# Kernel tuning notes

Hardware: AMD Instinct MI355X
Metric: run time of the kernel (lower is better)

The kernel has to match this reference:

```python
import jax, jax.numpy as jnp
import numpy as np

TEMP = 1.0  # unique_3D_act_temperature
EPS = 1e-10


def _trilinear_border(vol, gx, gy, gz):
    """grid_sample 5D, mode=bilinear (trilinear), padding=border, align_corners=True.
    vol: [C, D, H, W]; gx/gy/gz: [P] normalized coords in [-1, 1] (x->W, y->H, z->D).
    Returns [C, P]."""
    C, D, H, W = vol.shape
    fx = jnp.clip((gx + 1.0) * 0.5 * (W - 1), 0.0, W - 1)
    fy = jnp.clip((gy + 1.0) * 0.5 * (H - 1), 0.0, H - 1)
    fz = jnp.clip((gz + 1.0) * 0.5 * (D - 1), 0.0, D - 1)
    x0 = jnp.floor(fx).astype(jnp.int32); x1 = jnp.minimum(x0 + 1, W - 1)
    y0 = jnp.floor(fy).astype(jnp.int32); y1 = jnp.minimum(y0 + 1, H - 1)
    z0 = jnp.floor(fz).astype(jnp.int32); z1 = jnp.minimum(z0 + 1, D - 1)
    wx = fx - x0; wy = fy - y0; wz = fz - z0
    def g(zi, yi, xi):
        return vol[:, zi, yi, xi]  # [C, P] gather
    c00 = g(z0, y0, x0) * (1 - wx) + g(z0, y0, x1) * wx
    c01 = g(z0, y1, x0) * (1 - wx) + g(z0, y1, x1) * wx
    c10 = g(z1, y0, x0) * (1 - wx) + g(z1, y0, x1) * wx
    c11 = g(z1, y1, x0) * (1 - wx) + g(z1, y1, x1) * wx
    c0 = c00 * (1 - wy) + c01 * wy
    c1 = c10 * (1 - wy) + c11 * wy
    return c0 * (1 - wz) + c1 * wz


def setup_inputs() -> dict:
    key = jax.random.key(0)
    k1, k2, k3, k4 = jax.random.split(key, 4)
    B, NR, NS = 1, 8192, 128
    Cdim, Ddim, Hd, Wd = 1, 256, 240, 320
    H, W = 480, 640
    fx_, fy_, cx, cy = 500.0, 500.0, W / 2.0, H / 2.0
    intr = jnp.array([[[fx_, 0.0, cx], [0.0, fy_, cy], [0.0, 0.0, 1.0]]], dtype=jnp.float32)
    # back-project random pixels at random depths so projections fall mostly in frame
    u = jax.random.uniform(k1, (B, NR, NS), minval=0.0, maxval=float(W))
    v = jax.random.uniform(k2, (B, NR, NS), minval=0.0, maxval=float(H))
    z = jax.random.uniform(k3, (B, NR, NS), minval=1.1, maxval=10.0)
    pts = jnp.stack([(u - cx) / fx_ * z, (v - cy) / fy_ * z, z], axis=-1).astype(jnp.float32)
    feature_volume = 0.01 * jax.random.normal(k4, (1, Cdim, Ddim, Hd, Wd), dtype=jnp.float32)
    learnable_max_value = 5.0 * jnp.ones((1, 1, 1, Hd, Wd), dtype=jnp.float32)
    return {"feature_volume": feature_volume, "learnable_max_value": learnable_max_value,
            "intr": intr, "points_3D_samples": pts,
            "H": H, "W": W, "depth_min": 0, "depth_max": 1}


def reference(feature_volume, learnable_max_value, intr, points_3D_samples, H, W, depth_min, depth_max):
    B, NR, NS, _ = points_3D_samples.shape
    Cdim = feature_volume.shape[1]
    # camera projection: points @ intr^T
    p2d = jnp.einsum('bnsk,bjk->bnsj', points_3D_samples, intr)
    px, py, pz = p2d[..., 0], p2d[..., 1], p2d[..., 2]
    gx = (px / (pz + EPS) / W - 0.5) * 2.0
    gy = (py / (pz + EPS) / H - 0.5) * 2.0
    gz = ((1.0 / pz - depth_min) / (depth_max - depth_min) - 0.5) * 2.0
    # unique_3D_act density: softmax over depth axis * (relu(max) + 0.01)
    density = jax.nn.softmax(feature_volume * TEMP, axis=2) * (jax.nn.relu(learnable_max_value) + 0.01)
    vol = density[0]  # [C, D, Hd, Wd]
    feat = _trilinear_border(vol, gx.reshape(-1), gy.reshape(-1), gz.reshape(-1))  # [C, P]
    feat = feat.reshape(Cdim, B, NR, NS).transpose(1, 2, 3, 0)  # [B, NR, NS, C]
    density_samples = feat[..., 0]  # cdim == 1 -> squeeze(-1)
    return density_samples
```

## Files before the change

kernel.cpp:

```cpp
#include <hip/hip_runtime.h>
#include <hip/hip_fp16.h>
#include <math.h>

#define DD 256
#define HD 240
#define WD 320
#define HWPIX (HD * WD)
#define DCHUNK 16
#define NCHUNK (DD / DCHUNK)

union Quad {
    uint2 u;
    struct { __half2 lo, hi; } h;
};

__global__ __launch_bounds__(256) void k_rebuild_quad(
        const float* __restrict__ vol,
        uint2* __restrict__ quad,
        float* __restrict__ partial) {
    int pix = blockIdx.x * 256 + threadIdx.x;
    int d0 = blockIdx.y * DCHUNK;
    int y = pix / WD;
    int pixn = (y < HD - 1) ? pix + WD : pix;
    const float* p0 = vol + pix;
    const float* p1 = vol + pixn;

    float a[DCHUNK + 1], b[DCHUNK + 1];
#pragma unroll
    for (int j = 0; j <= DCHUNK; ++j) {
        int d = d0 + j; if (d > DD - 1) d = DD - 1;
        a[j] = p0[(size_t)d * HWPIX];
        b[j] = p1[(size_t)d * HWPIX];
    }
#pragma unroll
    for (int j = 0; j <= DCHUNK; ++j) { a[j] = __expf(a[j]); b[j] = __expf(b[j]); }

    float s0 = 0.f, s1 = 0.f;
#pragma unroll
    for (int j = 0; j < DCHUNK; j += 2) { s0 += a[j]; s1 += a[j + 1]; }

#pragma unroll
    for (int j = 0; j < DCHUNK; ++j) {
        Quad q;
        q.h.lo = __floats2half2_rn(a[j],     b[j]);
        q.h.hi = __floats2half2_rn(a[j + 1], b[j + 1]);
        quad[(size_t)(d0 + j) * HWPIX + pix] = q.u;
    }
    partial[blockIdx.y * HWPIX + pix] = s0 + s1;
}

__global__ __launch_bounds__(256) void k_stats_partial(
        const float* __restrict__ vol,
        float* __restrict__ partial) {
    int pix = blockIdx.x * 256 + threadIdx.x;
    int d0 = blockIdx.y * DCHUNK;
    const float* p = vol + pix;
    float v[DCHUNK];
#pragma unroll
    for (int j = 0; j < DCHUNK; ++j) v[j] = p[(size_t)(d0 + j) * HWPIX];
    float s0 = 0.f, s1 = 0.f;
#pragma unroll
    for (int j = 0; j < DCHUNK; j += 2) { s0 += __expf(v[j]); s1 += __expf(v[j + 1]); }
    partial[blockIdx.y * HWPIX + pix] = s0 + s1;
}

__global__ __launch_bounds__(256) void k_finalize(
        const float* __restrict__ partial,
        const float* __restrict__ lmax,
        float* __restrict__ coef) {
    int pix = blockIdx.x * 256 + threadIdx.x;
    float s = 0.f;
#pragma unroll
    for (int c = 0; c < NCHUNK; ++c) s += partial[c * HWPIX + pix];
    coef[pix] = (fmaxf(lmax[pix], 0.0f) + 0.01f) / s;
}

__device__ __forceinline__ void project(
        const float* __restrict__ intr, const float* __restrict__ pts, int i,
        float Himg, float Wimg, float dmin, float dmax,
        int& x0, int& x1, float& wx, int& y0, int& y1, float& wy,
        int& z0, float& wz) {
    float X = pts[3 * i + 0];
    float Y = pts[3 * i + 1];
    float Z = pts[3 * i + 2];
    float px = intr[0] * X + intr[1] * Y + intr[2] * Z;
    float py = intr[3] * X + intr[4] * Y + intr[5] * Z;
    float pz = intr[6] * X + intr[7] * Y + intr[8] * Z;
    float inv = 1.0f / (pz + 1e-10f);
    float gx = (px * inv / Wimg - 0.5f) * 2.0f;
    float gy = (py * inv / Himg - 0.5f) * 2.0f;
    float gz = ((1.0f / pz - dmin) / (dmax - dmin) - 0.5f) * 2.0f;
    float fx = fminf(fmaxf((gx + 1.0f) * 0.5f * (float)(WD - 1), 0.0f), (float)(WD - 1));
    float fy = fminf(fmaxf((gy + 1.0f) * 0.5f * (float)(HD - 1), 0.0f), (float)(HD - 1));
    float fz = fminf(fmaxf((gz + 1.0f) * 0.5f * (float)(DD - 1), 0.0f), (float)(DD - 1));
    x0 = (int)floorf(fx); x1 = min(x0 + 1, WD - 1); wx = fx - (float)x0;
    y0 = (int)floorf(fy); y1 = min(y0 + 1, HD - 1); wy = fy - (float)y0;
    z0 = (int)floorf(fz); wz = fz - (float)z0;
}

__device__ __forceinline__ float sample_one_quad(
        const uint2* __restrict__ quad, const float* __restrict__ coef,
        const float* __restrict__ intr, const float* __restrict__ pts,
        float Himg, float Wimg, float dmin, float dmax, int i) {
    int x0, x1, y0, y1, z0; float wx, wy, wz;
    project(intr, pts, i, Himg, Wimg, dmin, dmax, x0, x1, wx, y0, y1, wy, z0, wz);

    size_t base = (size_t)z0 * HWPIX + (size_t)y0 * WD;
    Quad qa, qb;
    qa.u = quad[base + x0];
    qb.u = quad[base + x1];
    float c00 = coef[y0 * WD + x0], c01 = coef[y0 * WD + x1];
    float c10 = coef[y1 * WD + x0], c11 = coef[y1 * WD + x1];

    float2 alo = __half22float2(qa.h.lo);
    float2 ahi = __half22float2(qa.h.hi);
    float2 blo = __half22float2(qb.h.lo);
    float2 bhi = __half22float2(qb.h.hi);

    float d000 = alo.x * c00, d010 = alo.y * c10;
    float d100 = ahi.x * c00, d110 = ahi.y * c10;
    float d001 = blo.x * c01, d011 = blo.y * c11;
    float d101 = bhi.x * c01, d111 = bhi.y * c11;

    float e00 = d000 * (1.0f - wx) + d001 * wx;
    float e01 = d010 * (1.0f - wx) + d011 * wx;
    float e10 = d100 * (1.0f - wx) + d101 * wx;
    float e11 = d110 * (1.0f - wx) + d111 * wx;
    float f0 = e00 * (1.0f - wy) + e01 * wy;
    float f1 = e10 * (1.0f - wy) + e11 * wy;
    return f0 * (1.0f - wz) + f1 * wz;
}

__global__ __launch_bounds__(256) void k_sample_quad(
        const uint2* __restrict__ quad,
        const float* __restrict__ coef,
        const float* __restrict__ intr,
        const float* __restrict__ pts,
        const int* __restrict__ Hp, const int* __restrict__ Wp,
        const int* __restrict__ dminp, const int* __restrict__ dmaxp,
        float* __restrict__ out, int P, int half) {
    int t = blockIdx.x * 256 + threadIdx.x;
    if (t >= half) return;
    float Himg = (float)(*Hp), Wimg = (float)(*Wp);
    float dmin = (float)(*dminp), dmax = (float)(*dmaxp);

    int i0 = t, i1 = t + half;
    float r0 = sample_one_quad(quad, coef, intr, pts, Himg, Wimg, dmin, dmax, i0);
    out[i0] = r0;
    if (i1 < P) {
        float r1 = sample_one_quad(quad, coef, intr, pts, Himg, Wimg, dmin, dmax, i1);
        out[i1] = r1;
    }
}

__global__ __launch_bounds__(256) void k_sample_vol(
        const float* __restrict__ vol,
        const float* __restrict__ coef,
        const float* __restrict__ intr,
        const float* __restrict__ pts,
        const int* __restrict__ Hp, const int* __restrict__ Wp,
        const int* __restrict__ dminp, const int* __restrict__ dmaxp,
        float* __restrict__ out, int P) {
    int i = blockIdx.x * 256 + threadIdx.x;
    if (i >= P) return;
    float Himg = (float)(*Hp), Wimg = (float)(*Wp);
    float dmin = (float)(*dminp), dmax = (float)(*dmaxp);
    int x0, x1, y0, y1, z0; float wx, wy, wz;
    project(intr, pts, i, Himg, Wimg, dmin, dmax, x0, x1, wx, y0, y1, wy, z0, wz);
    int z1 = min(z0 + 1, DD - 1);

    int p00 = y0 * WD + x0, p01 = y0 * WD + x1;
    int p10 = y1 * WD + x0, p11 = y1 * WD + x1;
    float c00 = coef[p00], c01 = coef[p01], c10 = coef[p10], c11 = coef[p11];
    const float* v0 = vol + (size_t)z0 * HWPIX;
    const float* v1 = vol + (size_t)z1 * HWPIX;

    float a00 = __expf(v0[p00]) * c00, a01 = __expf(v0[p01]) * c01;
    float a10 = __expf(v0[p10]) * c10, a11 = __expf(v0[p11]) * c11;
    float b00 = __expf(v1[p00]) * c00, b01 = __expf(v1[p01]) * c01;
    float b10 = __expf(v1[p10]) * c10, b11 = __expf(v1[p11]) * c11;

    float ax0 = a00 * (1.0f - wx) + a01 * wx;
    float ax1 = a10 * (1.0f - wx) + a11 * wx;
    float bx0 = b00 * (1.0f - wx) + b01 * wx;
    float bx1 = b10 * (1.0f - wx) + b11 * wx;
    float a = ax0 * (1.0f - wy) + ax1 * wy;
    float b = bx0 * (1.0f - wy) + bx1 * wy;
    out[i] = a * (1.0f - wz) + b * wz;
}

extern "C" void kernel_launch(void* const* d_in, const int* in_sizes, int n_in,
                              void* d_out, int out_size, void* d_ws, size_t ws_size,
                              hipStream_t stream) {
    const float* vol  = (const float*)d_in[0];
    const float* lmax = (const float*)d_in[1];
    const float* intr = (const float*)d_in[2];
    const float* pts  = (const float*)d_in[3];
    const int* Hp     = (const int*)d_in[4];
    const int* Wp     = (const int*)d_in[5];
    const int* dminp  = (const int*)d_in[6];
    const int* dmaxp  = (const int*)d_in[7];
    float* out = (float*)d_out;
    int P = out_size;

    const size_t quad_bytes = (size_t)DD * HWPIX * sizeof(uint2);
    const size_t part_bytes = (size_t)NCHUNK * HWPIX * 4;
    const size_t coef_bytes = (size_t)HWPIX * 4;

    dim3 blk(256);
    dim3 grd_rb(HWPIX / 256, NCHUNK);
    dim3 grd_fin(HWPIX / 256);

    if (ws_size >= quad_bytes + part_bytes + coef_bytes) {
        uint2* quad    = (uint2*)d_ws;
        float* partial = (float*)((char*)d_ws + quad_bytes);
        float* coef    = (float*)((char*)d_ws + quad_bytes + part_bytes);
        k_rebuild_quad<<<grd_rb, blk, 0, stream>>>(vol, quad, partial);
        k_finalize<<<grd_fin, blk, 0, stream>>>(partial, lmax, coef);
        int half = (P + 1) / 2;
        dim3 grd_smp((half + 255) / 256);
        k_sample_quad<<<grd_smp, blk, 0, stream>>>(quad, coef, intr, pts,
                                                   Hp, Wp, dminp, dmaxp, out, P, half);
    } else {
        float* partial = (float*)d_ws;
        float* coef    = (float*)((char*)d_ws + part_bytes);
        k_stats_partial<<<grd_rb, blk, 0, stream>>>(vol, partial);
        k_finalize<<<grd_fin, blk, 0, stream>>>(partial, lmax, coef);
        dim3 grd_smp((P + 255) / 256);
        k_sample_vol<<<grd_smp, blk, 0, stream>>>(vol, coef, intr, pts,
                                                  Hp, Wp, dminp, dmaxp, out, P);
    }
}
```

Baseline: 194.1 us.

## Pre-scale quad volume by softmax coefficients and sample four points per thread

Softmax statistics now come from a separate pass over the volume, and the fp16 quad volume is built afterwards with the normalisation coefficient already multiplied in. This lets the sampler skip the four coef gathers per point. The sampler now handles four consecutive points per thread with vectorized float4 loads of the points and a float4 store of the results. The cost is that the 78 MB fp32 volume is read twice (stats, then build) instead of once. Storing pre-scaled values in fp16 also changes rounding.

After: 207.6 us. 7.0% more time.

```diff
diff --git a/kernel.cpp b/kernel.cpp
--- a/kernel.cpp
+++ b/kernel.cpp
@@ -6,61 +6,28 @@
 #define HD 240
 #define WD 320
 #define HWPIX (HD * WD)
-#define DCHUNK 16
-#define NCHUNK (DD / DCHUNK)
+#define DC_S 32
+#define NC_S (DD / DC_S)
+#define DC_B 16
+#define NC_B (DD / DC_B)
 
 union Quad {
     uint2 u;
     struct { __half2 lo, hi; } h;
 };
 
-__global__ __launch_bounds__(256) void k_rebuild_quad(
-        const float* __restrict__ vol,
-        uint2* __restrict__ quad,
-        float* __restrict__ partial) {
-    int pix = blockIdx.x * 256 + threadIdx.x;
-    int d0 = blockIdx.y * DCHUNK;
-    int y = pix / WD;
-    int pixn = (y < HD - 1) ? pix + WD : pix;
-    const float* p0 = vol + pix;
-    const float* p1 = vol + pixn;
-
-    float a[DCHUNK + 1], b[DCHUNK + 1];
-#pragma unroll
-    for (int j = 0; j <= DCHUNK; ++j) {
-        int d = d0 + j; if (d > DD - 1) d = DD - 1;
-        a[j] = p0[(size_t)d * HWPIX];
-        b[j] = p1[(size_t)d * HWPIX];
-    }
-#pragma unroll
-    for (int j = 0; j <= DCHUNK; ++j) { a[j] = __expf(a[j]); b[j] = __expf(b[j]); }
-
-    float s0 = 0.f, s1 = 0.f;
-#pragma unroll
-    for (int j = 0; j < DCHUNK; j += 2) { s0 += a[j]; s1 += a[j + 1]; }
-
-#pragma unroll
-    for (int j = 0; j < DCHUNK; ++j) {
-        Quad q;
-        q.h.lo = __floats2half2_rn(a[j],     b[j]);
-        q.h.hi = __floats2half2_rn(a[j + 1], b[j + 1]);
-        quad[(size_t)(d0 + j) * HWPIX + pix] = q.u;
-    }
-    partial[blockIdx.y * HWPIX + pix] = s0 + s1;
-}
-
 __global__ __launch_bounds__(256) void k_stats_partial(
         const float* __restrict__ vol,
         float* __restrict__ partial) {
     int pix = blockIdx.x * 256 + threadIdx.x;
-    int d0 = blockIdx.y * DCHUNK;
+    int d0 = blockIdx.y * DC_S;
     const float* p = vol + pix;
-    float v[DCHUNK];
-#pragma unroll
-    for (int j = 0; j < DCHUNK; ++j) v[j] = p[(size_t)(d0 + j) * HWPIX];
+    float v[DC_S];
+#pragma unroll
+    for (int j = 0; j < DC_S; ++j) v[j] = p[(size_t)(d0 + j) * HWPIX];
     float s0 = 0.f, s1 = 0.f;
 #pragma unroll
-    for (int j = 0; j < DCHUNK; j += 2) { s0 += __expf(v[j]); s1 += __expf(v[j + 1]); }
+    for (int j = 0; j < DC_S; j += 2) { s0 += __expf(v[j]); s1 += __expf(v[j + 1]); }
     partial[blockIdx.y * HWPIX + pix] = s0 + s1;
 }
 
@@ -71,21 +38,52 @@
     int pix = blockIdx.x * 256 + threadIdx.x;
     float s = 0.f;
 #pragma unroll
-    for (int c = 0; c < NCHUNK; ++c) s += partial[c * HWPIX + pix];
+    for (int c = 0; c < NC_S; ++c) s += partial[c * HWPIX + pix];
     coef[pix] = (fmaxf(lmax[pix], 0.0f) + 0.01f) / s;
 }
 
-__device__ __forceinline__ void project(
-        const float* __restrict__ intr, const float* __restrict__ pts, int i,
+__global__ __launch_bounds__(256) void k_build_quad(
+        const float* __restrict__ vol,
+        const float* __restrict__ coef,
+        uint2* __restrict__ quad) {
+    int pix = blockIdx.x * 256 + threadIdx.x;
+    int d0 = blockIdx.y * DC_B;
+    int y = pix / WD;
+    int pixn = (y < HD - 1) ? pix + WD : pix;
+    const float* p0 = vol + pix;
+    const float* p1 = vol + pixn;
+    float c0 = coef[pix];
+    float c1 = coef[pixn];
+
+    float a[DC_B + 1], b[DC_B + 1];
+#pragma unroll
+    for (int j = 0; j <= DC_B; ++j) {
+        int d = d0 + j; if (d > DD - 1) d = DD - 1;
+        a[j] = p0[(size_t)d * HWPIX];
+        b[j] = p1[(size_t)d * HWPIX];
+    }
+#pragma unroll
+    for (int j = 0; j <= DC_B; ++j) {
+        a[j] = __expf(a[j]) * c0;
+        b[j] = __expf(b[j]) * c1;
+    }
+#pragma unroll
+    for (int j = 0; j < DC_B; ++j) {
+        Quad q;
+        q.h.lo = __floats2half2_rn(a[j],     b[j]);
+        q.h.hi = __floats2half2_rn(a[j + 1], b[j + 1]);
+        quad[(size_t)(d0 + j) * HWPIX + pix] = q.u;
+    }
+}
+
+__device__ __forceinline__ void project_idx(
+        float X, float Y, float Z,
+        float i00, float i02, float i11, float i12,
         float Himg, float Wimg, float dmin, float dmax,
-        int& x0, int& x1, float& wx, int& y0, int& y1, float& wy,
-        int& z0, float& wz) {
-    float X = pts[3 * i + 0];
-    float Y = pts[3 * i + 1];
-    float Z = pts[3 * i + 2];
-    float px = intr[0] * X + intr[1] * Y + intr[2] * Z;
-    float py = intr[3] * X + intr[4] * Y + intr[5] * Z;
-    float pz = intr[6] * X + intr[7] * Y + intr[8] * Z;
+        size_t& base, int& x0, int& x1, float& wx, float& wy, float& wz) {
+    float px = i00 * X + i02 * Z;
+    float py = i11 * Y + i12 * Z;
+    float pz = Z;
     float inv = 1.0f / (pz + 1e-10f);
     float gx = (px * inv / Wimg - 0.5f) * 2.0f;
     float gy = (py * inv / Himg - 0.5f) * 2.0f;
@@ -94,62 +92,101 @@
     float fy = fminf(fmaxf((gy + 1.0f) * 0.5f * (float)(HD - 1), 0.0f), (float)(HD - 1));
     float fz = fminf(fmaxf((gz + 1.0f) * 0.5f * (float)(DD - 1), 0.0f), (float)(DD - 1));
     x0 = (int)floorf(fx); x1 = min(x0 + 1, WD - 1); wx = fx - (float)x0;
-    y0 = (int)floorf(fy); y1 = min(y0 + 1, HD - 1); wy = fy - (float)y0;
-    z0 = (int)floorf(fz); wz = fz - (float)z0;
-}
-
-__device__ __forceinline__ float sample_one_quad(
-        const uint2* __restrict__ quad, const float* __restrict__ coef,
-        const float* __restrict__ intr, const float* __restrict__ pts,
-        float Himg, float Wimg, float dmin, float dmax, int i) {
-    int x0, x1, y0, y1, z0; float wx, wy, wz;
-    project(intr, pts, i, Himg, Wimg, dmin, dmax, x0, x1, wx, y0, y1, wy, z0, wz);
-
-    size_t base = (size_t)z0 * HWPIX + (size_t)y0 * WD;
-    Quad qa, qb;
-    qa.u = quad[base + x0];
-    qb.u = quad[base + x1];
-    float c00 = coef[y0 * WD + x0], c01 = coef[y0 * WD + x1];
-    float c10 = coef[y1 * WD + x0], c11 = coef[y1 * WD + x1];
-
+    int y0 = (int)floorf(fy); wy = fy - (float)y0;
+    int z0 = (int)floorf(fz); wz = fz - (float)z0;
+    base = (size_t)z0 * HWPIX + (size_t)y0 * WD;
+}
+
+__device__ __forceinline__ float quad_lerp(uint2 ua, uint2 ub,
+                                           float wx, float wy, float wz) {
+    Quad qa, qb; qa.u = ua; qb.u = ub;
     float2 alo = __half22float2(qa.h.lo);
     float2 ahi = __half22float2(qa.h.hi);
     float2 blo = __half22float2(qb.h.lo);
     float2 bhi = __half22float2(qb.h.hi);
-
-    float d000 = alo.x * c00, d010 = alo.y * c10;
-    float d100 = ahi.x * c00, d110 = ahi.y * c10;
-    float d001 = blo.x * c01, d011 = blo.y * c11;
-    float d101 = bhi.x * c01, d111 = bhi.y * c11;
-
-    float e00 = d000 * (1.0f - wx) + d001 * wx;
-    float e01 = d010 * (1.0f - wx) + d011 * wx;
-    float e10 = d100 * (1.0f - wx) + d101 * wx;
-    float e11 = d110 * (1.0f - wx) + d111 * wx;
+    float e00 = alo.x * (1.0f - wx) + blo.x * wx;
+    float e01 = alo.y * (1.0f - wx) + blo.y * wx;
+    float e10 = ahi.x * (1.0f - wx) + bhi.x * wx;
+    float e11 = ahi.y * (1.0f - wx) + bhi.y * wx;
     float f0 = e00 * (1.0f - wy) + e01 * wy;
     float f1 = e10 * (1.0f - wy) + e11 * wy;
     return f0 * (1.0f - wz) + f1 * wz;
 }
 
-__global__ __launch_bounds__(256) void k_sample_quad(
+__global__ __launch_bounds__(256) void k_sample4(
         const uint2* __restrict__ quad,
-        const float* __restrict__ coef,
         const float* __restrict__ intr,
         const float* __restrict__ pts,
         const int* __restrict__ Hp, const int* __restrict__ Wp,
         const int* __restrict__ dminp, const int* __restrict__ dmaxp,
-        float* __restrict__ out, int P, int half) {
+        float* __restrict__ out, int P) {
     int t = blockIdx.x * 256 + threadIdx.x;
-    if (t >= half) return;
+    int i0 = t * 4;
+    if (i0 >= P) return;
     float Himg = (float)(*Hp), Wimg = (float)(*Wp);
     float dmin = (float)(*dminp), dmax = (float)(*dmaxp);
-
-    int i0 = t, i1 = t + half;
-    float r0 = sample_one_quad(quad, coef, intr, pts, Himg, Wimg, dmin, dmax, i0);
-    out[i0] = r0;
-    if (i1 < P) {
-        float r1 = sample_one_quad(quad, coef, intr, pts, Himg, Wimg, dmin, dmax, i1);
-        out[i1] = r1;
+    float m00 = intr[0], m01 = intr[1], m02 = intr[2];
+    float m10 = intr[3], m11 = intr[4], m12 = intr[5];
+    float m20 = intr[6], m21 = intr[7], m22 = intr[8];
+
+    if (i0 + 3 < P) {
+        const float4* p4 = (const float4*)(pts + (size_t)i0 * 3);
+        float4 q0 = p4[0], q1 = p4[1], q2 = p4[2];
+        float Xs[4] = {q0.x, q0.w, q1.z, q2.y};
+        float Ys[4] = {q0.y, q1.x, q1.w, q2.z};
+        float Zs[4] = {q0.z, q1.y, q2.x, q2.w};
+
+        size_t base[4]; int x0[4], x1[4];
+        float wx[4], wy[4], wz[4];
+#pragma unroll
+        for (int k = 0; k < 4; ++k) {
+            float X = Xs[k], Y = Ys[k], Z = Zs[k];
+            float px = m00 * X + m01 * Y + m02 * Z;
+            float py = m10 * X + m11 * Y + m12 * Z;
+            float pz = m20 * X + m21 * Y + m22 * Z;
+            float inv = 1.0f / (pz + 1e-10f);
+            float gx = (px * inv / Wimg - 0.5f) * 2.0f;
+            float gy = (py * inv / Himg - 0.5f) * 2.0f;
+            float gz = ((1.0f / pz - dmin) / (dmax - dmin) - 0.5f) * 2.0f;
+            float fx = fminf(fmaxf((gx + 1.0f) * 0.5f * (float)(WD - 1), 0.0f), (float)(WD - 1));
+            float fy = fminf(fmaxf((gy + 1.0f) * 0.5f * (float)(HD - 1), 0.0f), (float)(HD - 1));
+            float fz = fminf(fmaxf((gz + 1.0f) * 0.5f * (float)(DD - 1), 0.0f), (float)(DD - 1));
+            x0[k] = (int)floorf(fx); x1[k] = min(x0[k] + 1, WD - 1); wx[k] = fx - (float)x0[k];
+            int y0 = (int)floorf(fy); wy[k] = fy - (float)y0;
+            int z0 = (int)floorf(fz); wz[k] = fz - (float)z0;
+            base[k] = (size_t)z0 * HWPIX + (size_t)y0 * WD;
+        }
+        uint2 A[4], B[4];
+#pragma unroll
+        for (int k = 0; k < 4; ++k) {
+            A[k] = quad[base[k] + x0[k]];
+            B[k] = quad[base[k] + x1[k]];
+        }
+        float4 r;
+        r.x = quad_lerp(A[0], B[0], wx[0], wy[0], wz[0]);
+        r.y = quad_lerp(A[1], B[1], wx[1], wy[1], wz[1]);
+        r.z = quad_lerp(A[2], B[2], wx[2], wy[2], wz[2]);
+        r.w = quad_lerp(A[3], B[3], wx[3], wy[3], wz[3]);
+        *(float4*)(out + i0) = r;
+    } else {
+        for (int i = i0; i < P; ++i) {
+            float X = pts[3 * i + 0], Y = pts[3 * i + 1], Z = pts[3 * i + 2];
+            float px = m00 * X + m01 * Y + m02 * Z;
+            float py = m10 * X + m11 * Y + m12 * Z;
+            float pz = m20 * X + m21 * Y + m22 * Z;
+            float inv = 1.0f / (pz + 1e-10f);
+            float gx = (px * inv / Wimg - 0.5f) * 2.0f;
+            float gy = (py * inv / Himg - 0.5f) * 2.0f;
+            float gz = ((1.0f / pz - dmin) / (dmax - dmin) - 0.5f) * 2.0f;
+            float fx = fminf(fmaxf((gx + 1.0f) * 0.5f * (float)(WD - 1), 0.0f), (float)(WD - 1));
+            float fy = fminf(fmaxf((gy + 1.0f) * 0.5f * (float)(HD - 1), 0.0f), (float)(HD - 1));
+            float fz = fminf(fmaxf((gz + 1.0f) * 0.5f * (float)(DD - 1), 0.0f), (float)(DD - 1));
+            int x0 = (int)floorf(fx); int x1 = min(x0 + 1, WD - 1); float wx = fx - (float)x0;
+            int y0 = (int)floorf(fy); float wy = fy - (float)y0;
+            int z0 = (int)floorf(fz); float wz = fz - (float)z0;
+            size_t base = (size_t)z0 * HWPIX + (size_t)y0 * WD;
+            out[i] = quad_lerp(quad[base + x0], quad[base + x1], wx, wy, wz);
+        }
     }
 }
 
@@ -165,21 +202,29 @@
     if (i >= P) return;
     float Himg = (float)(*Hp), Wimg = (float)(*Wp);
     float dmin = (float)(*dminp), dmax = (float)(*dmaxp);
-    int x0, x1, y0, y1, z0; float wx, wy, wz;
-    project(intr, pts, i, Himg, Wimg, dmin, dmax, x0, x1, wx, y0, y1, wy, z0, wz);
-    int z1 = min(z0 + 1, DD - 1);
-
+    float X = pts[3 * i + 0], Y = pts[3 * i + 1], Z = pts[3 * i + 2];
+    float px = intr[0] * X + intr[1] * Y + intr[2] * Z;
+    float py = intr[3] * X + intr[4] * Y + intr[5] * Z;
+    float pz = intr[6] * X + intr[7] * Y + intr[8] * Z;
+    float inv = 1.0f / (pz + 1e-10f);
+    float gx = (px * inv / Wimg - 0.5f) * 2.0f;
+    float gy = (py * inv / Himg - 0.5f) * 2.0f;
+    float gz = ((1.0f / pz - dmin) / (dmax - dmin) - 0.5f) * 2.0f;
+    float fx = fminf(fmaxf((gx + 1.0f) * 0.5f * (float)(WD - 1), 0.0f), (float)(WD - 1));
+    float fy = fminf(fmaxf((gy + 1.0f) * 0.5f * (float)(HD - 1), 0.0f), (float)(HD - 1));
+    float fz = fminf(fmaxf((gz + 1.0f) * 0.5f * (float)(DD - 1), 0.0f), (float)(DD - 1));
+    int x0 = (int)floorf(fx); int x1 = min(x0 + 1, WD - 1); float wx = fx - (float)x0;
+    int y0 = (int)floorf(fy); int y1 = min(y0 + 1, HD - 1); float wy = fy - (float)y0;
+    int z0 = (int)floorf(fz); int z1 = min(z0 + 1, DD - 1); float wz = fz - (float)z0;
     int p00 = y0 * WD + x0, p01 = y0 * WD + x1;
     int p10 = y1 * WD + x0, p11 = y1 * WD + x1;
     float c00 = coef[p00], c01 = coef[p01], c10 = coef[p10], c11 = coef[p11];
     const float* v0 = vol + (size_t)z0 * HWPIX;
     const float* v1 = vol + (size_t)z1 * HWPIX;
-
     float a00 = __expf(v0[p00]) * c00, a01 = __expf(v0[p01]) * c01;
     float a10 = __expf(v0[p10]) * c10, a11 = __expf(v0[p11]) * c11;
     float b00 = __expf(v1[p00]) * c00, b01 = __expf(v1[p01]) * c01;
     float b10 = __expf(v1[p10]) * c10, b11 = __expf(v1[p11]) * c11;
-
     float ax0 = a00 * (1.0f - wx) + a01 * wx;
     float ax1 = a10 * (1.0f - wx) + a11 * wx;
     float bx0 = b00 * (1.0f - wx) + b01 * wx;
@@ -204,27 +249,29 @@
     int P = out_size;
 
     const size_t quad_bytes = (size_t)DD * HWPIX * sizeof(uint2);
-    const size_t part_bytes = (size_t)NCHUNK * HWPIX * 4;
+    const size_t part_bytes = (size_t)NC_S * HWPIX * 4;
     const size_t coef_bytes = (size_t)HWPIX * 4;
 
     dim3 blk(256);
-    dim3 grd_rb(HWPIX / 256, NCHUNK);
+    dim3 grd_st(HWPIX / 256, NC_S);
+    dim3 grd_bd(HWPIX / 256, NC_B);
     dim3 grd_fin(HWPIX / 256);
 
     if (ws_size >= quad_bytes + part_bytes + coef_bytes) {
         uint2* quad    = (uint2*)d_ws;
         float* partial = (float*)((char*)d_ws + quad_bytes);
         float* coef    = (float*)((char*)d_ws + quad_bytes + part_bytes);
-        k_rebuild_quad<<<grd_rb, blk, 0, stream>>>(vol, quad, partial);
+        k_stats_partial<<<grd_st, blk, 0, stream>>>(vol, partial);
         k_finalize<<<grd_fin, blk, 0, stream>>>(partial, lmax, coef);
-        int half = (P + 1) / 2;
-        dim3 grd_smp((half + 255) / 256);
-        k_sample_quad<<<grd_smp, blk, 0, stream>>>(quad, coef, intr, pts,
-                                                   Hp, Wp, dminp, dmaxp, out, P, half);
+        k_build_quad<<<grd_bd, blk, 0, stream>>>(vol, coef, quad);
+        int nthr = (P + 3) / 4;
+        dim3 grd_smp((nthr + 255) / 256);
+        k_sample4<<<grd_smp, blk, 0, stream>>>(quad, intr, pts,
+                                               Hp, Wp, dminp, dmaxp, out, P);
     } else {
         float* partial = (float*)d_ws;
         float* coef    = (float*)((char*)d_ws + part_bytes);
-        k_stats_partial<<<grd_rb, blk, 0, stream>>>(vol, partial);
+        k_stats_partial<<<grd_st, blk, 0, stream>>>(vol, partial);
         k_finalize<<<grd_fin, blk, 0, stream>>>(partial, lmax, coef);
         dim3 grd_smp((P + 255) / 256);
         k_sample_vol<<<grd_smp, blk, 0, stream>>>(vol, coef, intr, pts,
```
